# Kernel tuning notes

Measured on AMD Instinct MI355X. Metric: run time of the kernel, lower is better.

Reference implementation:

```python
import jax, jax.numpy as jnp
import numpy as np

B, T, I, H, L = 256, 2000, 80, 20, 2
G = 4 * H  # gates i,f,g,o (PyTorch order)


def _lstm_dir(xg, w_hh, reverse):
    # xg: [B, T, 4H] precomputed input-gate contributions (incl. bias)
    # w_hh: [H, 4H]
    xg_t = jnp.swapaxes(xg, 0, 1)  # [T, B, 4H]
    if reverse:
        xg_t = xg_t[::-1]

    def step(carry, g_x):
        h, c = carry
        gates = g_x + h @ w_hh  # [B, 4H]
        i, f, g, o = jnp.split(gates, 4, axis=-1)
        c = jax.nn.sigmoid(f) * c + jax.nn.sigmoid(i) * jnp.tanh(g)
        h = jax.nn.sigmoid(o) * jnp.tanh(c)
        return (h, c), h

    h0 = jnp.zeros((xg.shape[0], H), xg.dtype)
    _, hs = jax.lax.scan(step, (h0, h0), xg_t)  # hs: [T, B, H]
    if reverse:
        hs = hs[::-1]
    return jnp.swapaxes(hs, 0, 1)  # [B, T, H]


def _bilstm_layer(x, w_ih, w_hh, b):
    # x: [B, T, in], w_ih: [2, in, 4H], w_hh: [2, H, 4H], b: [2, 4H]
    out = []
    for d in range(2):
        xg = jnp.einsum('bti,ig->btg', x, w_ih[d]) + b[d]
        out.append(_lstm_dir(xg, w_hh[d], reverse=(d == 1)))
    return jnp.concatenate(out, axis=-1)  # [B, T, 2H]


def setup_inputs() -> dict:
    key = jax.random.key(0)
    ks = jax.random.split(key, 9)
    s = 1.0 / np.sqrt(H)
    u = lambda k, shp: jax.random.uniform(k, shp, jnp.float32, -s, s)
    return {
        'x': jax.random.normal(ks[0], (B, T, I), jnp.float32),
        'w_ih_l0': u(ks[1], (2, I, G)),
        'w_hh_l0': u(ks[2], (2, H, G)),
        'b_l0': u(ks[3], (2, G)),
        'w_ih_l1': u(ks[4], (2, 2 * H, G)),
        'w_hh_l1': u(ks[5], (2, H, G)),
        'b_l1': u(ks[6], (2, G)),
        'fc_w': u(ks[7], (1, 2 * H)),
        'fc_b': u(ks[8], (1,)),
    }


def reference(x, w_ih_l0, w_hh_l0, b_l0, w_ih_l1, w_hh_l1, b_l1, fc_w, fc_b):
    h = _bilstm_layer(x, w_ih_l0, w_hh_l0, b_l0)      # [B, T, 2H]
    h = _bilstm_layer(h, w_ih_l1, w_hh_l1, b_l1)      # [B, T, 2H]
    out = h @ fc_w.T + fc_b                           # [B, T, 1]
    return out.squeeze(-1)                            # [B, T]
```

## Files before the change

kernel.cpp:

```cpp
#include <hip/hip_runtime.h>
#include <math.h>

#define B_ 256
#define T_ 2000
#define I_ 80
#define H_ 20
#define G_ 80
#define M_ 512000

#define LOG2E 1.442695041f

typedef __attribute__((ext_vector_type(2))) float f32x2;
typedef __attribute__((ext_vector_type(2))) unsigned u32x2;

__device__ __forceinline__ f32x2 mk2(float a, float b) { f32x2 r; r.x = a; r.y = b; return r; }

__device__ __forceinline__ float swap_half(float x, int swapidx) {
#if __has_builtin(__builtin_amdgcn_permlane32_swap)
    u32x2 r = __builtin_amdgcn_permlane32_swap(__float_as_uint(x), __float_as_uint(x), false, false);
    return __uint_as_float(r.y);
#else
    (void)0;
    return __uint_as_float((unsigned)__builtin_amdgcn_ds_bpermute(swapidx, (int)__float_as_uint(x)));
#endif
}

template<int K>
__global__ __launch_bounds__(256) void gemm_xg(
    const float* __restrict__ X,
    const float* __restrict__ Wih,
    const float* __restrict__ Bias,
    float* __restrict__ XG,
    int M)
{
    constexpr int KC = 40;
    __shared__ float ws[KC][164];
    __shared__ float xs[KC][100];
    __shared__ float bs[160];

    const int tid  = threadIdx.x;
    const int row0 = blockIdx.x * 96;
    const int tx = tid % 20;
    const int ty = tid / 20;
    const bool run = (ty < 12);

    if (tid < 160) {
        int dd = (tid >= 80);
        int r = tid - 80 * dd;
        int j = r >> 2, g = r & 3;
        float sc = (g == 2) ? 2.0f * LOG2E : -LOG2E;
        bs[tid] = sc * Bias[dd * 80 + g * 20 + j];
    }

    int nrows = M - row0; if (nrows > 96) nrows = 96;

    float acc[8][8];
    bool first = true;

    for (int kc = 0; kc < K; kc += KC) {
        for (int idx = tid; idx < KC * 160; idx += 256) {
            int i = idx / 160, cc = idx - 160 * i;
            int dd = (cc >= 80), r = cc - 80 * dd;
            int j = r >> 2, g = r & 3;
            float sc = (g == 2) ? 2.0f * LOG2E : -LOG2E;
            ws[i][cc] = sc * Wih[(dd * K + kc + i) * 80 + g * 20 + j];
        }
        for (int i4 = tid; i4 < (96 * KC) / 4; i4 += 256) {
            int r = i4 / 10;
            int kk = (i4 - 10 * r) * 4;
            float4 v = make_float4(0.f, 0.f, 0.f, 0.f);
            if (r < nrows)
                v = *(const float4*)(X + (long long)(row0 + r) * K + kc + kk);
            xs[kk][r] = v.x; xs[kk + 1][r] = v.y; xs[kk + 2][r] = v.z; xs[kk + 3][r] = v.w;
        }
        __syncthreads();

        if (first) {
            first = false;
            float bv[8];
            #pragma unroll
            for (int cc = 0; cc < 8; ++cc) bv[cc] = bs[tx * 8 + cc];
            #pragma unroll
            for (int r = 0; r < 8; ++r)
                #pragma unroll
                for (int cc = 0; cc < 8; ++cc) acc[r][cc] = bv[cc];
        }

        if (run) {
            #pragma unroll 4
            for (int k = 0; k < KC; ++k) {
                float a[8], bb[8];
                *(float4*)&a[0]  = *(const float4*)&xs[k][ty * 8];
                *(float4*)&a[4]  = *(const float4*)&xs[k][ty * 8 + 4];
                *(float4*)&bb[0] = *(const float4*)&ws[k][tx * 8];
                *(float4*)&bb[4] = *(const float4*)&ws[k][tx * 8 + 4];
                #pragma unroll
                for (int r = 0; r < 8; ++r)
                    #pragma unroll
                    for (int cc = 0; cc < 8; ++cc)
                        acc[r][cc] = fmaf(a[r], bb[cc], acc[r][cc]);
            }
        }
        __syncthreads();
    }

    if (run) {
        #pragma unroll
        for (int r = 0; r < 8; ++r) {
            int row = row0 + ty * 8 + r;
            if (row < M) {
                float* dst = XG + (long long)row * 160 + tx * 8;
                *(float4*)(dst)     = *(float4*)&acc[r][0];
                *(float4*)(dst + 4) = *(float4*)&acc[r][4];
            }
        }
    }
}

__global__ __launch_bounds__(256) void gemm_xg_tA(
    const float* __restrict__ H0t,
    const float* __restrict__ Wih,
    const float* __restrict__ Bias,
    float* __restrict__ XG,
    int T)
{
    constexpr int K = 40;
    __shared__ float ws[K][164];
    __shared__ float xs[K][100];
    __shared__ float bs[160];

    const int tid = threadIdx.x;
    const int bb  = blockIdx.x / 21;
    const int tc  = blockIdx.x % 21;
    const int t0  = tc * 96;
    const int tx  = tid % 20;
    const int ty  = tid / 20;
    const bool run = (ty < 12);

    if (tid < 160) {
        int dd = (tid >= 80);
        int r = tid - 80 * dd;
        int j = r >> 2, g = r & 3;
        float sc = (g == 2) ? 2.0f * LOG2E : -LOG2E;
        bs[tid] = sc * Bias[dd * 80 + g * 20 + j];
    }

    int nrows = T - t0; if (nrows > 96) nrows = 96;

    for (int idx = tid; idx < K * 160; idx += 256) {
        int i = idx / 160, cc = idx - 160 * i;
        int dd = (cc >= 80), r = cc - 80 * dd;
        int j = r >> 2, g = r & 3;
        float sc = (g == 2) ? 2.0f * LOG2E : -LOG2E;
        ws[i][cc] = sc * Wih[(dd * K + i) * 80 + g * 20 + j];
    }
    for (int i4 = tid; i4 < K * 24; i4 += 256) {
        int k = i4 / 24;
        int r = (i4 - 24 * k) * 4;
        float4 v = make_float4(0.f, 0.f, 0.f, 0.f);
        if (r < nrows)
            v = *(const float4*)(H0t + ((long long)bb * 40 + k) * T + t0 + r);
        *(float4*)&xs[k][r] = v;
    }
    __syncthreads();

    float acc[8][8];
    {
        float bv[8];
        #pragma unroll
        for (int cc = 0; cc < 8; ++cc) bv[cc] = bs[tx * 8 + cc];
        #pragma unroll
        for (int r = 0; r < 8; ++r)
            #pragma unroll
            for (int cc = 0; cc < 8; ++cc) acc[r][cc] = bv[cc];
    }

    if (run) {
        #pragma unroll 4
        for (int k = 0; k < K; ++k) {
            float a[8], bb2[8];
            *(float4*)&a[0]   = *(const float4*)&xs[k][ty * 8];
            *(float4*)&a[4]   = *(const float4*)&xs[k][ty * 8 + 4];
            *(float4*)&bb2[0] = *(const float4*)&ws[k][tx * 8];
            *(float4*)&bb2[4] = *(const float4*)&ws[k][tx * 8 + 4];
            #pragma unroll
            for (int r = 0; r < 8; ++r)
                #pragma unroll
                for (int cc = 0; cc < 8; ++cc)
                    acc[r][cc] = fmaf(a[r], bb2[cc], acc[r][cc]);
        }

        #pragma unroll
        for (int r = 0; r < 8; ++r) {
            int rr = ty * 8 + r;
            if (rr < nrows) {
                long long row = (long long)bb * T + t0 + rr;
                float* dst = XG + row * 160 + tx * 8;
                *(float4*)(dst)     = *(float4*)&acc[r][0];
                *(float4*)(dst + 4) = *(float4*)&acc[r][4];
            }
        }
    }
}

__attribute__((amdgpu_waves_per_eu(1, 1)))
__global__ __launch_bounds__(64) void lstm_scan(
    const float* __restrict__ xg,
    const float* __restrict__ w_hh,
    float* __restrict__ h_out,
    int T)
{
    const int bd   = blockIdx.x;
    const int b    = bd >> 1;
    const int d    = bd & 1;
    const int lane = threadIdx.x & 63;
    const int half = lane >> 5;
    const int j    = lane & 31;
    const bool act_lane = (lane < H_);
    const int jj   = (j < H_) ? j : 0;
    const bool isB = (d == 1);

    const int swapidx = ((lane + 32) & 63) << 2;

    const int gA = half ? 2 : 0;
    const int gB = gA + 1;
    const float scA = half ? (2.0f * LOG2E) : (-LOG2E);
    const float scB = -LOG2E;

    f32x2 wA[10], wB[10];
    const float* wb = w_hh + d * (H_ * G_);
    #pragma unroll
    for (int i = 0; i < 10; ++i) {
        wA[i] = mk2(scA * wb[(2 * i) * G_ + gA * 20 + jj],
                    scA * wb[(2 * i + 1) * G_ + gA * 20 + jj]);
        wB[i] = mk2(scB * wb[(2 * i) * G_ + gB * 20 + jj],
                    scB * wb[(2 * i + 1) * G_ + gB * 20 + jj]);
    }

    float sh[20];
    #pragma unroll
    for (int k = 0; k < 20; ++k) sh[k] = 0.f;
    float c = 0.f;

    const int t0    = isB ? (T - 1) : 0;
    const int rstep = isB ? -160 : 160;
    const float* pf = xg + ((long long)(b * T + t0) * 2 + d) * 80 + 4 * jj + 2 * half;

    float* hp = h_out + ((long long)b * 40 + d * 20 + jj) * T + (isB ? T - 4 : 0);
    const int hgstep = isB ? -4 : 4;

    constexpr int PF = 8;
    f32x2 px[PF];
    #pragma unroll
    for (int s = 0; s < PF; ++s) { px[s] = *(const f32x2*)pf; pf += rstep; }

    float hq0 = 0.f, hq1 = 0.f, hq2 = 0.f, hq3 = 0.f;

    for (int tb = 0; tb < T; tb += PF) {
        #pragma unroll
        for (int s = 0; s < PF; ++s) {
            const f32x2 v = px[s];
            px[s] = *(const f32x2*)pf; pf += rstep;

            f32x2 aA1 = mk2(v.x, 0.f);
            f32x2 aA2 = mk2(0.f, 0.f);
            f32x2 aB1 = mk2(v.y, 0.f);
            f32x2 aB2 = mk2(0.f, 0.f);
            #pragma unroll
            for (int i = 0; i < 5; ++i) {
                const f32x2 hlo = mk2(sh[2 * i],      sh[2 * i + 1]);
                const f32x2 hhi = mk2(sh[10 + 2 * i], sh[11 + 2 * i]);
                aA1 = __builtin_elementwise_fma(wA[i],     hlo, aA1);
                aA2 = __builtin_elementwise_fma(wA[i + 5], hhi, aA2);
                aB1 = __builtin_elementwise_fma(wB[i],     hlo, aB1);
                aB2 = __builtin_elementwise_fma(wB[i + 5], hhi, aB2);
            }
            const f32x2 tA = aA1 + aA2;
            const f32x2 tB = aB1 + aB2;
            const float mA = tA.x + tA.y;
            const float mB = tB.x + tB.y;

            const float sA = __builtin_amdgcn_rcpf(1.0f + __builtin_amdgcn_exp2f(mA));
            const float sB = __builtin_amdgcn_rcpf(1.0f + __builtin_amdgcn_exp2f(mB));

            const float sAx = swap_half(sA, swapidx);
            const float gox = swap_half(sB, swapidx);

            const float gg = fmaf(-2.0f, sAx, 1.0f);
            c = fmaf(sB, c, sA * gg);
            const float th = fmaf(-2.0f,
                __builtin_amdgcn_rcpf(1.0f + __builtin_amdgcn_exp2f(2.0f * LOG2E * c)), 1.0f);
            const float hj = gox * th;

            {
                const int p = s & 3;
                if (p == 0) hq0 = hj;
                else if (p == 1) hq1 = hj;
                else if (p == 2) hq2 = hj;
                else {
                    hq3 = hj;
                    float4 sv;
                    sv.x = isB ? hq3 : hq0;
                    sv.y = isB ? hq2 : hq1;
                    sv.z = isB ? hq1 : hq2;
                    sv.w = isB ? hq0 : hq3;
                    if (act_lane) *(float4*)hp = sv;
                    hp += hgstep;
                }
            }

            #pragma unroll
            for (int k = 0; k < 20; ++k)
                sh[k] = __uint_as_float(__builtin_amdgcn_readlane(__float_as_uint(hj), k));
        }
    }
}

__global__ __launch_bounds__(256) void fc_t(
    const float* __restrict__ H1t,
    const float* __restrict__ Wf,
    const float* __restrict__ Bf,
    float* __restrict__ Out,
    int T)
{
    const int b   = blockIdx.x;
    const int t   = blockIdx.y * 1024 + threadIdx.x * 4;
    if (t > T - 4) return;

    const float bias = Bf[0];
    float4 acc = make_float4(bias, bias, bias, bias);
    const float* base = H1t + (long long)b * 40 * T + t;
    #pragma unroll 8
    for (int u = 0; u < 40; ++u) {
        const float wv = Wf[u];
        const float4 hv = *(const float4*)(base + (long long)u * T);
        acc.x = fmaf(hv.x, wv, acc.x);
        acc.y = fmaf(hv.y, wv, acc.y);
        acc.z = fmaf(hv.z, wv, acc.z);
        acc.w = fmaf(hv.w, wv, acc.w);
    }
    *(float4*)(Out + (long long)b * T + t) = acc;
}

extern "C" void kernel_launch(void* const* d_in, const int* in_sizes, int n_in,
                              void* d_out, int out_size, void* d_ws, size_t ws_size,
                              hipStream_t stream) {
    const float* x     = (const float*)d_in[0];
    const float* wih0  = (const float*)d_in[1];
    const float* whh0  = (const float*)d_in[2];
    const float* b0    = (const float*)d_in[3];
    const float* wih1  = (const float*)d_in[4];
    const float* whh1  = (const float*)d_in[5];
    const float* b1    = (const float*)d_in[6];
    const float* fcw   = (const float*)d_in[7];
    const float* fcb   = (const float*)d_in[8];
    float* out = (float*)d_out;

    float* ws = (float*)d_ws;
    float* xg  = ws + 2048;
    float* h0t = xg + 81920000LL + 2048;
    float* h1t = h0t + 20480000LL;

    const int M = M_;
    const int gemm_grid = (M + 95) / 96;

    gemm_xg<80><<<dim3(gemm_grid), dim3(256), 0, stream>>>(x, wih0, b0, xg, M);
    lstm_scan<<<dim3(B_ * 2), dim3(64), 0, stream>>>(xg, whh0, h0t, T_);
    gemm_xg_tA<<<dim3(B_ * 21), dim3(256), 0, stream>>>(h0t, wih1, b1, xg, T_);
    lstm_scan<<<dim3(B_ * 2), dim3(64), 0, stream>>>(xg, whh1, h1t, T_);
    fc_t<<<dim3(B_, 2), dim3(256), 0, stream>>>(h1t, fcw, fcb, out, T_);
}
```

Measured before the change: 1.343 ms.

## Process both LSTM directions in one wavefront to interleave independent recurrences

The scan kernel now handles the forward and reverse directions of a batch element in the same wave and launches half as many blocks. The two independent recurrence chains are interleaved so their dependent latencies (readlane broadcasts, transcendental ops, cross-half swaps) can overlap. In exchange each wave issues twice the instructions per step and uses more registers, and half the waves are available to spread across SIMDs.

```diff
diff --git a/kernel.cpp b/kernel.cpp
--- a/kernel.cpp
+++ b/kernel.cpp
@@ -20,7 +20,6 @@
     u32x2 r = __builtin_amdgcn_permlane32_swap(__float_as_uint(x), __float_as_uint(x), false, false);
     return __uint_as_float(r.y);
 #else
-    (void)0;
     return __uint_as_float((unsigned)__builtin_amdgcn_ds_bpermute(swapidx, (int)__float_as_uint(x)));
 #endif
 }
@@ -210,15 +209,12 @@
     float* __restrict__ h_out,
     int T)
 {
-    const int bd   = blockIdx.x;
-    const int b    = bd >> 1;
-    const int d    = bd & 1;
+    const int b    = blockIdx.x;
     const int lane = threadIdx.x & 63;
     const int half = lane >> 5;
     const int j    = lane & 31;
     const bool act_lane = (lane < H_);
     const int jj   = (j < H_) ? j : 0;
-    const bool isB = (d == 1);
 
     const int swapidx = ((lane + 32) & 63) << 2;
 
@@ -227,91 +223,126 @@
     const float scA = half ? (2.0f * LOG2E) : (-LOG2E);
     const float scB = -LOG2E;
 
-    f32x2 wA[10], wB[10];
-    const float* wb = w_hh + d * (H_ * G_);
+    f32x2 wAF[10], wBF[10], wAR[10], wBR[10];
+    {
+        const float* wbF = w_hh;
+        const float* wbR = w_hh + H_ * G_;
+        #pragma unroll
+        for (int i = 0; i < 10; ++i) {
+            wAF[i] = mk2(scA * wbF[(2 * i) * G_ + gA * 20 + jj],
+                         scA * wbF[(2 * i + 1) * G_ + gA * 20 + jj]);
+            wBF[i] = mk2(scB * wbF[(2 * i) * G_ + gB * 20 + jj],
+                         scB * wbF[(2 * i + 1) * G_ + gB * 20 + jj]);
+            wAR[i] = mk2(scA * wbR[(2 * i) * G_ + gA * 20 + jj],
+                         scA * wbR[(2 * i + 1) * G_ + gA * 20 + jj]);
+            wBR[i] = mk2(scB * wbR[(2 * i) * G_ + gB * 20 + jj],
+                         scB * wbR[(2 * i + 1) * G_ + gB * 20 + jj]);
+        }
+    }
+
+    float shF[20], shR[20];
     #pragma unroll
-    for (int i = 0; i < 10; ++i) {
-        wA[i] = mk2(scA * wb[(2 * i) * G_ + gA * 20 + jj],
-                    scA * wb[(2 * i + 1) * G_ + gA * 20 + jj]);
-        wB[i] = mk2(scB * wb[(2 * i) * G_ + gB * 20 + jj],
-                    scB * wb[(2 * i + 1) * G_ + gB * 20 + jj]);
-    }
-
-    float sh[20];
+    for (int k = 0; k < 20; ++k) { shF[k] = 0.f; shR[k] = 0.f; }
+    float cF = 0.f, cR = 0.f;
+
+    const float* pfF = xg + ((long long)(b * T) * 2 + 0) * 80 + 4 * jj + 2 * half;
+    const float* pfR = xg + ((long long)(b * T + T - 1) * 2 + 1) * 80 + 4 * jj + 2 * half;
+
+    float* hpF = h_out + ((long long)b * 40 + jj) * T;
+    float* hpR = h_out + ((long long)b * 40 + 20 + jj) * T + (T - 4);
+
+    constexpr int PF = 8;
+    f32x2 pxF[PF], pxR[PF];
     #pragma unroll
-    for (int k = 0; k < 20; ++k) sh[k] = 0.f;
-    float c = 0.f;
-
-    const int t0    = isB ? (T - 1) : 0;
-    const int rstep = isB ? -160 : 160;
-    const float* pf = xg + ((long long)(b * T + t0) * 2 + d) * 80 + 4 * jj + 2 * half;
-
-    float* hp = h_out + ((long long)b * 40 + d * 20 + jj) * T + (isB ? T - 4 : 0);
-    const int hgstep = isB ? -4 : 4;
-
-    constexpr int PF = 8;
-    f32x2 px[PF];
-    #pragma unroll
-    for (int s = 0; s < PF; ++s) { px[s] = *(const f32x2*)pf; pf += rstep; }
-
-    float hq0 = 0.f, hq1 = 0.f, hq2 = 0.f, hq3 = 0.f;
+    for (int s = 0; s < PF; ++s) {
+        pxF[s] = *(const f32x2*)pfF; pfF += 160;
+        pxR[s] = *(const f32x2*)pfR; pfR -= 160;
+    }
+
+    float hqF0 = 0.f, hqF1 = 0.f, hqF2 = 0.f, hqF3 = 0.f;
+    float hqR0 = 0.f, hqR1 = 0.f, hqR2 = 0.f, hqR3 = 0.f;
 
     for (int tb = 0; tb < T; tb += PF) {
         #pragma unroll
         for (int s = 0; s < PF; ++s) {
-            const f32x2 v = px[s];
-            px[s] = *(const f32x2*)pf; pf += rstep;
-
-            f32x2 aA1 = mk2(v.x, 0.f);
-            f32x2 aA2 = mk2(0.f, 0.f);
-            f32x2 aB1 = mk2(v.y, 0.f);
-            f32x2 aB2 = mk2(0.f, 0.f);
+            const f32x2 vF = pxF[s];
+            pxF[s] = *(const f32x2*)pfF; pfF += 160;
+            const f32x2 vR = pxR[s];
+            pxR[s] = *(const f32x2*)pfR; pfR -= 160;
+
+            f32x2 aA1F = mk2(vF.x, 0.f), aA2F = mk2(0.f, 0.f);
+            f32x2 aB1F = mk2(vF.y, 0.f), aB2F = mk2(0.f, 0.f);
+            f32x2 aA1R = mk2(vR.x, 0.f), aA2R = mk2(0.f, 0.f);
+            f32x2 aB1R = mk2(vR.y, 0.f), aB2R = mk2(0.f, 0.f);
             #pragma unroll
             for (int i = 0; i < 5; ++i) {
-                const f32x2 hlo = mk2(sh[2 * i],      sh[2 * i + 1]);
-                const f32x2 hhi = mk2(sh[10 + 2 * i], sh[11 + 2 * i]);
-                aA1 = __builtin_elementwise_fma(wA[i],     hlo, aA1);
-                aA2 = __builtin_elementwise_fma(wA[i + 5], hhi, aA2);
-                aB1 = __builtin_elementwise_fma(wB[i],     hlo, aB1);
-                aB2 = __builtin_elementwise_fma(wB[i + 5], hhi, aB2);
-            }
-            const f32x2 tA = aA1 + aA2;
-            const f32x2 tB = aB1 + aB2;
-            const float mA = tA.x + tA.y;
-            const float mB = tB.x + tB.y;
-
-            const float sA = __builtin_amdgcn_rcpf(1.0f + __builtin_amdgcn_exp2f(mA));
-            const float sB = __builtin_amdgcn_rcpf(1.0f + __builtin_amdgcn_exp2f(mB));
-
-            const float sAx = swap_half(sA, swapidx);
-            const float gox = swap_half(sB, swapidx);
-
-            const float gg = fmaf(-2.0f, sAx, 1.0f);
-            c = fmaf(sB, c, sA * gg);
-            const float th = fmaf(-2.0f,
-                __builtin_amdgcn_rcpf(1.0f + __builtin_amdgcn_exp2f(2.0f * LOG2E * c)), 1.0f);
-            const float hj = gox * th;
+                const f32x2 hloF = mk2(shF[2 * i],      shF[2 * i + 1]);
+                const f32x2 hhiF = mk2(shF[10 + 2 * i], shF[11 + 2 * i]);
+                const f32x2 hloR = mk2(shR[2 * i],      shR[2 * i + 1]);
+                const f32x2 hhiR = mk2(shR[10 + 2 * i], shR[11 + 2 * i]);
+                aA1F = __builtin_elementwise_fma(wAF[i],     hloF, aA1F);
+                aA1R = __builtin_elementwise_fma(wAR[i],     hloR, aA1R);
+                aA2F = __builtin_elementwise_fma(wAF[i + 5], hhiF, aA2F);
+                aA2R = __builtin_elementwise_fma(wAR[i + 5], hhiR, aA2R);
+                aB1F = __builtin_elementwise_fma(wBF[i],     hloF, aB1F);
+                aB1R = __builtin_elementwise_fma(wBR[i],     hloR, aB1R);
+                aB2F = __builtin_elementwise_fma(wBF[i + 5], hhiF, aB2F);
+                aB2R = __builtin_elementwise_fma(wBR[i + 5], hhiR, aB2R);
+            }
+            const f32x2 tAF = aA1F + aA2F;
+            const f32x2 tBF = aB1F + aB2F;
+            const f32x2 tAR = aA1R + aA2R;
+            const f32x2 tBR = aB1R + aB2R;
+            const float mAF = tAF.x + tAF.y;
+            const float mBF = tBF.x + tBF.y;
+            const float mAR = tAR.x + tAR.y;
+            const float mBR = tBR.x + tBR.y;
+
+            const float sAF = __builtin_amdgcn_rcpf(1.0f + __builtin_amdgcn_exp2f(mAF));
+            const float sBF = __builtin_amdgcn_rcpf(1.0f + __builtin_amdgcn_exp2f(mBF));
+            const float sAR = __builtin_amdgcn_rcpf(1.0f + __builtin_amdgcn_exp2f(mAR));
+            const float sBR = __builtin_amdgcn_rcpf(1.0f + __builtin_amdgcn_exp2f(mBR));
+
+            const float sAxF = swap_half(sAF, swapidx);
+            const float goxF = swap_half(sBF, swapidx);
+            const float sAxR = swap_half(sAR, swapidx);
+            const float goxR = swap_half(sBR, swapidx);
+
+            const float ggF = fmaf(-2.0f, sAxF, 1.0f);
+            const float ggR = fmaf(-2.0f, sAxR, 1.0f);
+            cF = fmaf(sBF, cF, sAF * ggF);
+            cR = fmaf(sBR, cR, sAR * ggR);
+            const float thF = fmaf(-2.0f,
+                __builtin_amdgcn_rcpf(1.0f + __builtin_amdgcn_exp2f(2.0f * LOG2E * cF)), 1.0f);
+            const float thR = fmaf(-2.0f,
+                __builtin_amdgcn_rcpf(1.0f + __builtin_amdgcn_exp2f(2.0f * LOG2E * cR)), 1.0f);
+            const float hjF = goxF * thF;
+            const float hjR = goxR * thR;
 
             {
                 const int p = s & 3;
-                if (p == 0) hq0 = hj;
-                else if (p == 1) hq1 = hj;
-                else if (p == 2) hq2 = hj;
+                if (p == 0) { hqF0 = hjF; hqR0 = hjR; }
+                else if (p == 1) { hqF1 = hjF; hqR1 = hjR; }
+                else if (p == 2) { hqF2 = hjF; hqR2 = hjR; }
                 else {
-                    hq3 = hj;
-                    float4 sv;
-                    sv.x = isB ? hq3 : hq0;
-                    sv.y = isB ? hq2 : hq1;
-                    sv.z = isB ? hq1 : hq2;
-                    sv.w = isB ? hq0 : hq3;
-                    if (act_lane) *(float4*)hp = sv;
-                    hp += hgstep;
+                    hqF3 = hjF; hqR3 = hjR;
+                    float4 svF, svR;
+                    svF.x = hqF0; svF.y = hqF1; svF.z = hqF2; svF.w = hqF3;
+                    svR.x = hqR3; svR.y = hqR2; svR.z = hqR1; svR.w = hqR0;
+                    if (act_lane) {
+                        *(float4*)hpF = svF;
+                        *(float4*)hpR = svR;
+                    }
+                    hpF += 4;
+                    hpR -= 4;
                 }
             }
 
             #pragma unroll
-            for (int k = 0; k < 20; ++k)
-                sh[k] = __uint_as_float(__builtin_amdgcn_readlane(__float_as_uint(hj), k));
+            for (int k = 0; k < 20; ++k) {
+                shF[k] = __uint_as_float(__builtin_amdgcn_readlane(__float_as_uint(hjF), k));
+                shR[k] = __uint_as_float(__builtin_amdgcn_readlane(__float_as_uint(hjR), k));
+            }
         }
     }
 }
@@ -365,8 +396,8 @@
     const int gemm_grid = (M + 95) / 96;
 
     gemm_xg<80><<<dim3(gemm_grid), dim3(256), 0, stream>>>(x, wih0, b0, xg, M);
-    lstm_scan<<<dim3(B_ * 2), dim3(64), 0, stream>>>(xg, whh0, h0t, T_);
+    lstm_scan<<<dim3(B_), dim3(64), 0, stream>>>(xg, whh0, h0t, T_);
     gemm_xg_tA<<<dim3(B_ * 21), dim3(256), 0, stream>>>(h0t, wih1, b1, xg, T_);
-    lstm_scan<<<dim3(B_ * 2), dim3(64), 0, stream>>>(xg, whh1, h1t, T_);
+    lstm_scan<<<dim3(B_), dim3(64), 0, stream>>>(xg, whh1, h1t, T_);
     fc_t<<<dim3(B_, 2), dim3(256), 0, stream>>>(h1t, fcw, fcb, out, T_);
 }
```

After: 1.759 ms. +30.9%, slower.
